# Optimization experiments

Measured on AMD Instinct MI355X. Metric: run time of the kernel, lower is better.

Reference implementation:

```python
import jax, jax.numpy as jnp
import numpy as np

D_MODEL, N_HEADS, WINDOW, N_STATE = 1024, 16, 256, 128
B, T = 2, 2048
EPS = 1e-5


def _layernorm(x, g, b):
    mu = jnp.mean(x, axis=-1, keepdims=True)
    var = jnp.mean((x - mu) ** 2, axis=-1, keepdims=True)
    return (x - mu) * jax.lax.rsqrt(var + EPS) * g + b


def setup_inputs() -> dict:
    key = jax.random.key(0)
    ks = jax.random.split(key, 20)
    d, h = D_MODEL, 4 * D_MODEL
    s = lambda k, *shape: jax.random.normal(k, shape, jnp.float32) * 0.02
    return {
        "x": jax.random.normal(ks[0], (B, T, d), jnp.float32),
        "ssm_state": jnp.zeros((B, N_STATE), jnp.float32),
        "ln1_g": jnp.ones((d,), jnp.float32), "ln1_b": jnp.zeros((d,), jnp.float32),
        "wq": s(ks[1], d, d), "bq": jnp.zeros((d,), jnp.float32),
        "wk": s(ks[2], d, d), "bk": jnp.zeros((d,), jnp.float32),
        "wv": s(ks[3], d, d), "bv": jnp.zeros((d,), jnp.float32),
        "wo": s(ks[4], d, d), "bo": jnp.zeros((d,), jnp.float32),
        "wg": s(ks[5], d, d), "bg": jnp.zeros((d,), jnp.float32),
        "A": jax.random.uniform(ks[6], (N_STATE,), jnp.float32, -0.1, 0.1),
        "Bw": s(ks[7], d, N_STATE),
        "Cw": s(ks[8], N_STATE, d),
        "ln2_g": jnp.ones((d,), jnp.float32), "ln2_b": jnp.zeros((d,), jnp.float32),
        "w1": s(ks[9], d, h), "b1": jnp.zeros((h,), jnp.float32),
        "w2": s(ks[10], h, d), "b2": jnp.zeros((d,), jnp.float32),
    }


def _forward(x, ssm_state, ln1_g, ln1_b, wq, bq, wk, bk, wv, bv, wo, bo,
             wg, bg, A, Bw, Cw, ln2_g, ln2_b, w1, b1, w2, b2):
    Bsz, Tlen, d = x.shape
    d_h = d // N_HEADS
    xn = _layernorm(x, ln1_g, ln1_b)

    # --- windowed causal attention (dense, per original) ---
    def heads(y):
        return y.reshape(Bsz, Tlen, N_HEADS, d_h).transpose(0, 2, 1, 3)
    Q = heads(xn @ wq + bq)
    K = heads(xn @ wk + bk)
    V = heads(xn @ wv + bv)
    scores = jnp.einsum("bhqd,bhkd->bhqk", Q, K) / (d_h ** 0.5)
    i = jnp.arange(Tlen)[:, None]
    j = jnp.arange(Tlen)[None, :]
    allowed = (j <= i) & (i - j < WINDOW)
    scores = jnp.where(allowed, scores, -jnp.inf)
    attn = jax.nn.softmax(scores, axis=-1)
    ao = jnp.einsum("bhqk,bhkd->bhqd", attn, V)
    ao = ao.transpose(0, 2, 1, 3).reshape(Bsz, Tlen, d)
    attn_out = ao @ wo + bo

    # --- diagonal SSM scan ---
    u = xn @ Bw  # (B,T,N)
    def step(s, u_t):
        s = A * s + u_t
        return s, s
    new_state, states = jax.lax.scan(step, ssm_state, u.transpose(1, 0, 2))
    ssm_out = states.transpose(1, 0, 2) @ Cw  # (B,T,d)

    # --- gated fusion + residual + MLP ---
    g = jax.nn.sigmoid(xn @ wg + bg)
    x = x + g * attn_out + (1.0 - g) * ssm_out
    xn2 = _layernorm(x, ln2_g, ln2_b)
    mlp = jax.nn.gelu(xn2 @ w1 + b1, approximate=False) @ w2 + b2
    return x + mlp, new_state


def reference(x, ssm_state, ln1_g, ln1_b, wq, bq, wk, bk, wv, bv, wo, bo,
              wg, bg, A, Bw, Cw, ln2_g, ln2_b, w1, b1, w2, b2):
    return _forward(x, ssm_state, ln1_g, ln1_b, wq, bq, wk, bk, wv, bv, wo, bo,
                    wg, bg, A, Bw, Cw, ln2_g, ln2_b, w1, b1, w2, b2)
```

## Files before the change

### kernel.cpp

```cpp
#include <hip/hip_runtime.h>

typedef __attribute__((ext_vector_type(8))) short bf16x8;
typedef __attribute__((ext_vector_type(4))) float f32x4;

#define D_MODEL 1024
#define T_LEN 2048
#define BATCH 2
#define N_HEADS 16
#define D_HEAD 64
#define WINDOW 256
#define N_STATE 128
#define D_FF 4096
#define N_CAT 4224
#define LDQ 4352
#define M_ROWS 4096

static __device__ __forceinline__ float bf2f(unsigned short u) {
  union { unsigned int i; float f; } v; v.i = ((unsigned int)u) << 16; return v.f;
}
static __device__ __forceinline__ unsigned short f2bf(float f) {
  unsigned int x = __float_as_uint(f);
  return (unsigned short)((x + 0x7FFFu + ((x >> 16) & 1u)) >> 16);
}

static __device__ __forceinline__ void gl_lds16(const void* g, void* l) {
  __builtin_amdgcn_global_load_lds(
      (const __attribute__((address_space(1))) unsigned int*)g,
      (__attribute__((address_space(3))) unsigned int*)l, 16, 0, 0);
}

__global__ __launch_bounds__(256) void transpose_cvt(
    const float* __restrict__ src, unsigned short* __restrict__ dst,
    int K, int N, int n_off, int ldd)
{
  __shared__ float tile[32][33];
  const int kt = blockIdx.x * 32, nt = blockIdx.y * 32;
  const int c = threadIdx.x & 31, r0 = threadIdx.x >> 5;
#pragma unroll
  for (int i = 0; i < 4; i++) {
    const int r = r0 + i * 8;
    tile[r][c] = src[(size_t)(kt + r) * N + nt + c];
  }
  __syncthreads();
#pragma unroll
  for (int i = 0; i < 4; i++) {
    const int r = r0 + i * 8;
    dst[(size_t)(n_off + nt + r) * ldd + kt + c] = f2bf(tile[c][r]);
  }
}

__global__ __launch_bounds__(256) void transpose5(
    const float* __restrict__ s0, const float* __restrict__ s1,
    const float* __restrict__ s2, const float* __restrict__ s3,
    const float* __restrict__ s4, unsigned short* __restrict__ dcat,
    unsigned short* __restrict__ dwo)
{
  __shared__ float tile[32][33];
  const int z = blockIdx.z;
  const float* src = (z == 0) ? s0 : (z == 1) ? s1 : (z == 2) ? s2 : (z == 3) ? s3 : s4;
  unsigned short* dst = (z < 4) ? dcat + (size_t)z * 1024 * 1024 : dwo;
  const int kt = blockIdx.x * 32, nt = blockIdx.y * 32;
  const int c = threadIdx.x & 31, r0 = threadIdx.x >> 5;
#pragma unroll
  for (int i = 0; i < 4; i++) {
    const int r = r0 + i * 8;
    tile[r][c] = src[(size_t)(kt + r) * 1024 + nt + c];
  }
  __syncthreads();
#pragma unroll
  for (int i = 0; i < 4; i++) {
    const int r = r0 + i * 8;
    dst[(size_t)(nt + r) * 1024 + kt + c] = f2bf(tile[c][r]);
  }
}

__global__ __launch_bounds__(256) void vtrans_kernel(
    const unsigned short* __restrict__ qkvgu, unsigned short* __restrict__ VT)
{
  __shared__ unsigned short tile[32][33];
  const int bh = blockIdx.z;
  const int b = bh >> 4, h = bh & 15;
  const int t0 = blockIdx.x * 32, d0 = blockIdx.y * 32;
  const int c = threadIdx.x & 31, r0 = threadIdx.x >> 5;
#pragma unroll
  for (int i = 0; i < 4; i++) {
    const int r = r0 + i * 8;
    tile[r][c] = qkvgu[((size_t)b * T_LEN + t0 + r) * LDQ + 2048 + h * 64 + d0 + c];
  }
  __syncthreads();
#pragma unroll
  for (int i = 0; i < 4; i++) {
    const int r = r0 + i * 8;
    VT[((size_t)bh * 64 + d0 + r) * T_LEN + t0 + c] = tile[c][r];
  }
}

__global__ __launch_bounds__(256) void build_bcat(
    const float* __restrict__ bq, const float* __restrict__ bk,
    const float* __restrict__ bv, const float* __restrict__ bg,
    float* __restrict__ bcat)
{
  const int i = blockIdx.x * 256 + threadIdx.x;
  if (i < LDQ) {
    float v = 0.0f;
    if (i < 1024)      v = bq[i];
    else if (i < 2048) v = bk[i - 1024];
    else if (i < 3072) v = bv[i - 2048];
    else if (i < 4096) v = bg[i - 3072];
    bcat[i] = v;
  }
}

__global__ __launch_bounds__(256) void ln_kernel(
    const float* __restrict__ x, const float* __restrict__ g,
    const float* __restrict__ b, unsigned short* __restrict__ out)
{
  const int row = blockIdx.x, tid = threadIdx.x;
  const float4 xv = ((const float4*)(x + (size_t)row * 1024))[tid];
  float s  = xv.x + xv.y + xv.z + xv.w;
  float s2 = xv.x * xv.x + xv.y * xv.y + xv.z * xv.z + xv.w * xv.w;
#pragma unroll
  for (int off = 32; off >= 1; off >>= 1) {
    s  += __shfl_down(s, off);
    s2 += __shfl_down(s2, off);
  }
  __shared__ float red[8];
  const int wave = tid >> 6;
  if ((tid & 63) == 0) { red[wave] = s; red[4 + wave] = s2; }
  __syncthreads();
  s  = red[0] + red[1] + red[2] + red[3];
  s2 = red[4] + red[5] + red[6] + red[7];
  const float mu = s * (1.0f / 1024.0f);
  const float rs = rsqrtf(s2 * (1.0f / 1024.0f) - mu * mu + 1e-5f);
  const float4 gv = ((const float4*)g)[tid];
  const float4 bv = ((const float4*)b)[tid];
  ushort4 o;
  o.x = f2bf((xv.x - mu) * rs * gv.x + bv.x);
  o.y = f2bf((xv.y - mu) * rs * gv.y + bv.y);
  o.z = f2bf((xv.z - mu) * rs * gv.z + bv.z);
  o.w = f2bf((xv.w - mu) * rs * gv.w + bv.w);
  ((ushort4*)(out + (size_t)row * 1024))[tid] = o;
}

template<int ACT, bool OUT_BF16, bool RESID>
__global__ __launch_bounds__(256, 4) void gemm_ho(
    const unsigned short* __restrict__ A, const unsigned short* __restrict__ BT,
    const float* __restrict__ bias, const float* __restrict__ resid,
    void* __restrict__ Cout, int ldc, int K, int nbx)
{
  __shared__ char As[16384];
  __shared__ char Bs[8192];
  const int nwg = gridDim.x;
  int bid = blockIdx.x;
  {
    const int q = nwg >> 3, r = nwg & 7, xx = bid & 7, o = bid >> 3;
    bid = (xx < r ? xx * (q + 1) : r * (q + 1) + (xx - r) * q) + o;
  }
  const int m0 = (bid % nbx) * 128;
  const int n0 = (bid / nbx) * 64;
  const int tid = threadIdx.x, lane = tid & 63, wave = tid >> 6;
  const int l15 = lane & 15, lg = lane >> 4;
  const int wm = (wave & 1) * 64, wn = (wave >> 1) * 32;
  f32x4 acc[4][2];
#pragma unroll
  for (int i = 0; i < 4; i++)
#pragma unroll
    for (int j = 0; j < 2; j++) acc[i][j] = (f32x4){0.f, 0.f, 0.f, 0.f};

  const char* srcA[4]; const char* srcB[2];
#pragma unroll
  for (int j = 0; j < 4; j++) {
    const int p = j * 4096 + tid * 16;
    const int R = p >> 7;
    const int cb = (p & 127) ^ ((R & 7) << 4);
    srcA[j] = (const char*)A + (size_t)(m0 + R) * (size_t)(K * 2) + cb;
    if (j < 2) srcB[j] = (const char*)BT + (size_t)(n0 + R) * (size_t)(K * 2) + cb;
  }

  const int NT = K >> 6;
  for (int t = 0; t < NT; ++t) {
    __syncthreads();
#pragma unroll
    for (int j = 0; j < 4; j++)
      gl_lds16(srcA[j] + (size_t)t * 128, As + j * 4096 + tid * 16);
#pragma unroll
    for (int j = 0; j < 2; j++)
      gl_lds16(srcB[j] + (size_t)t * 128, Bs + j * 4096 + tid * 16);
    __syncthreads();
    bf16x8 af[4][2], bfr[2][2];
#pragma unroll
    for (int mf = 0; mf < 4; mf++)
#pragma unroll
      for (int ks = 0; ks < 2; ks++) {
        const int R = wm + mf * 16 + l15;
        af[mf][ks] = *(const bf16x8*)(As + (R << 7) + ((ks * 64 + lg * 16) ^ ((R & 7) << 4)));
      }
#pragma unroll
    for (int nf = 0; nf < 2; nf++)
#pragma unroll
      for (int ks = 0; ks < 2; ks++) {
        const int R = wn + nf * 16 + l15;
        bfr[nf][ks] = *(const bf16x8*)(Bs + (R << 7) + ((ks * 64 + lg * 16) ^ ((R & 7) << 4)));
      }
#pragma unroll
    for (int mf = 0; mf < 4; mf++)
#pragma unroll
      for (int nf = 0; nf < 2; nf++)
#pragma unroll
        for (int ks = 0; ks < 2; ks++)
          acc[mf][nf] = __builtin_amdgcn_mfma_f32_16x16x32_bf16(
              af[mf][ks], bfr[nf][ks], acc[mf][nf], 0, 0, 0);
  }

  if (OUT_BF16) {
    __syncthreads();
    unsigned short (*Ct)[64] = (unsigned short(*)[64])As;
#pragma unroll
    for (int nf = 0; nf < 2; nf++) {
      const int col = wn + nf * 16 + l15;
      const float bv = bias ? bias[n0 + col] : 0.0f;
#pragma unroll
      for (int mf = 0; mf < 4; mf++) {
        const int rbase = wm + mf * 16 + lg * 4;
#pragma unroll
        for (int r = 0; r < 4; r++) {
          float v = acc[mf][nf][r] + bv;
          if (ACT == 2) v = 0.5f * v * (1.0f + erff(v * 0.70710678118654752f));
          Ct[rbase + r][col] = f2bf(v);
        }
      }
    }
    __syncthreads();
    unsigned short* Cb = (unsigned short*)Cout;
#pragma unroll
    for (int pass = 0; pass < 4; pass++) {
      const int idx = pass * 256 + tid;
      const int row = idx >> 3, c8 = (idx & 7) * 8;
      const uint4 d = *(const uint4*)&Ct[row][c8];
      *(uint4*)(Cb + (size_t)(m0 + row) * ldc + n0 + c8) = d;
    }
  } else {
#pragma unroll
    for (int nf = 0; nf < 2; nf++) {
      const int col = n0 + wn + nf * 16 + l15;
      const float bv = bias ? bias[col] : 0.0f;
#pragma unroll
      for (int mf = 0; mf < 4; mf++) {
        const int rbase = m0 + wm + mf * 16 + lg * 4;
#pragma unroll
        for (int r = 0; r < 4; r++) {
          float v = acc[mf][nf][r] + bv;
          if (ACT == 2) v = 0.5f * v * (1.0f + erff(v * 0.70710678118654752f));
          const size_t idx = (size_t)(rbase + r) * ldc + col;
          if (RESID) v += resid[idx];
          ((float*)Cout)[idx] = v;
        }
      }
    }
  }
}

__global__ __launch_bounds__(256) void attn_kernel(
    const unsigned short* __restrict__ qkvgu, const unsigned short* __restrict__ VT,
    unsigned short* __restrict__ ao)
{
  __shared__ float S[16][276];
  unsigned short* P = (unsigned short*)&S[0][0];

  const int bx = ((blockIdx.x & 7) << 4) | (blockIdx.x >> 3);
  const int q0 = bx * 16;
  const int h  = blockIdx.y;
  const int b  = blockIdx.z;
  const int tid = threadIdx.x, lane = tid & 63, wave = tid >> 6;
  const int l15 = lane & 15, lg = lane >> 4;
  const size_t rowbase = (size_t)b * T_LEN;

  {
    const unsigned short* qp = qkvgu + (rowbase + q0 + l15) * LDQ + h * 64 + lg * 8;
    const bf16x8 aq0 = *(const bf16x8*)qp;
    const bf16x8 aq1 = *(const bf16x8*)(qp + 32);
    for (int kt = wave; kt < 17; kt += 4) {
      const int kbase = q0 - 256 + kt * 16;
      const int krow = kbase + l15;
      const int krc = krow < 0 ? 0 : krow;
      const unsigned short* kp = qkvgu + (rowbase + krc) * LDQ + 1024 + h * 64 + lg * 8;
      const bf16x8 bk0 = *(const bf16x8*)kp;
      const bf16x8 bk1 = *(const bf16x8*)(kp + 32);
      f32x4 sacc = (f32x4){0.f, 0.f, 0.f, 0.f};
      sacc = __builtin_amdgcn_mfma_f32_16x16x32_bf16(aq0, bk0, sacc, 0, 0, 0);
      sacc = __builtin_amdgcn_mfma_f32_16x16x32_bf16(aq1, bk1, sacc, 0, 0, 0);
#pragma unroll
      for (int r = 0; r < 4; r++) {
        const int qi = q0 + lg * 4 + r;
        const int kj = kbase + l15;
        const bool ok = (kj >= 0) && (kj <= qi) && (qi - kj < WINDOW);
        S[lg * 4 + r][kt * 16 + l15] = ok ? sacc[r] * 0.125f : -1e30f;
      }
    }
  }
  __syncthreads();

  {
    const int q = tid >> 4, sub = tid & 15;
    float mx = -1e30f;
    for (int c = sub; c < 272; c += 16) mx = fmaxf(mx, S[q][c]);
#pragma unroll
    for (int off = 8; off >= 1; off >>= 1) mx = fmaxf(mx, __shfl_xor(mx, off));
    float sum = 0.f;
    for (int c = sub; c < 272; c += 16) sum += __expf(S[q][c] - mx);
#pragma unroll
    for (int off = 8; off >= 1; off >>= 1) sum += __shfl_xor(sum, off);
    const float inv = 1.0f / sum;
    unsigned short* Prow = P + q * 552;
    for (int c = sub; c < 288; c += 16) {
      const float pv = (c < 272) ? __expf(S[q][c] - mx) * inv : 0.0f;
      Prow[c] = f2bf(pv);
    }
  }
  __syncthreads();

  {
    f32x4 oacc = (f32x4){0.f, 0.f, 0.f, 0.f};
    const int dn = wave * 16 + l15;
    const unsigned short* vrow = VT + ((size_t)(b * 16 + h) * 64 + dn) * T_LEN;
#pragma unroll
    for (int ks = 0; ks < 9; ks++) {
      const bf16x8 pa = *(const bf16x8*)(P + l15 * 552 + ks * 32 + lg * 8);
      int t = q0 - 256 + ks * 32 + lg * 8;
      t = t < 0 ? 0 : (t > T_LEN - 8 ? T_LEN - 8 : t);
      const bf16x8 vb = *(const bf16x8*)(vrow + t);
      oacc = __builtin_amdgcn_mfma_f32_16x16x32_bf16(pa, vb, oacc, 0, 0, 0);
    }
#pragma unroll
    for (int r = 0; r < 4; r++)
      ao[(rowbase + q0 + lg * 4 + r) * D_MODEL + h * 64 + dn] = f2bf(oacc[r]);
  }
}

__global__ __launch_bounds__(512) void scan_kernel(
    const unsigned short* __restrict__ qkvgu, const float* __restrict__ Avec,
    const float* __restrict__ s0, unsigned short* __restrict__ states,
    float* __restrict__ out_state)
{
  __shared__ float finals[8][128];
  const int b = blockIdx.x;
  const int tid = threadIdx.x;
  const int c = tid >> 6;
  const int n0 = (tid & 63) * 2;
  const float a0 = Avec[n0], a1 = Avec[n0 + 1];
  float sv0 = (c == 0) ? s0[b * 128 + n0]     : 0.0f;
  float sv1 = (c == 0) ? s0[b * 128 + n0 + 1] : 0.0f;
  const size_t ubase = (size_t)b * T_LEN * LDQ + 4096 + n0;
  unsigned short* sp = states + (size_t)b * T_LEN * N_STATE + n0;
  const int t0 = c * 256;
#pragma unroll 8
  for (int t = t0; t < t0 + 256; t++) {
    const ushort2 u = *(const ushort2*)&qkvgu[ubase + (size_t)t * LDQ];
    sv0 = fmaf(a0, sv0, bf2f(u.x));
    sv1 = fmaf(a1, sv1, bf2f(u.y));
    ushort2 o; o.x = f2bf(sv0); o.y = f2bf(sv1);
    *(ushort2*)&sp[(size_t)t * N_STATE] = o;
  }
  finals[c][n0] = sv0;
  finals[c][n0 + 1] = sv1;
  if (c == 7) { out_state[b * 128 + n0] = sv0; out_state[b * 128 + n0 + 1] = sv1; }
  __syncthreads();
  if (c > 0) {
    const float c0 = finals[c - 1][n0];
    const float c1 = finals[c - 1][n0 + 1];
    float f0 = a0, f1 = a1;
    for (int t = t0; t < t0 + 256; t++) {
      if (f0 == 0.0f && f1 == 0.0f) break;
      ushort2 cur = *(ushort2*)&sp[(size_t)t * N_STATE];
      cur.x = f2bf(bf2f(cur.x) + f0 * c0);
      cur.y = f2bf(bf2f(cur.y) + f1 * c1);
      *(ushort2*)&sp[(size_t)t * N_STATE] = cur;
      f0 *= a0; f1 *= a1;
    }
  }
}

__global__ __launch_bounds__(256) void fusion_ln2_kernel(
    const float* __restrict__ x, const unsigned short* __restrict__ qkvgu,
    const unsigned short* __restrict__ attn, const unsigned short* __restrict__ ssm,
    const float* __restrict__ g2, const float* __restrict__ b2,
    float* __restrict__ out, unsigned short* __restrict__ xn2)
{
  const int row = blockIdx.x, tid = threadIdx.x;
  const size_t e4 = (size_t)row * 1024 + tid * 4;
  const float4 xv = *(const float4*)(x + e4);
  const ushort4 au = *(const ushort4*)(attn + e4);
  const ushort4 su = *(const ushort4*)(ssm + e4);
  const ushort4 gu = *(const ushort4*)(qkvgu + (size_t)row * LDQ + 3072 + tid * 4);
  float4 o;
  {
    const float ga = 1.0f / (1.0f + __expf(-bf2f(gu.x)));
    const float gb = 1.0f / (1.0f + __expf(-bf2f(gu.y)));
    const float gc = 1.0f / (1.0f + __expf(-bf2f(gu.z)));
    const float gd = 1.0f / (1.0f + __expf(-bf2f(gu.w)));
    o.x = xv.x + ga * bf2f(au.x) + (1.0f - ga) * bf2f(su.x);
    o.y = xv.y + gb * bf2f(au.y) + (1.0f - gb) * bf2f(su.y);
    o.z = xv.z + gc * bf2f(au.z) + (1.0f - gc) * bf2f(su.z);
    o.w = xv.w + gd * bf2f(au.w) + (1.0f - gd) * bf2f(su.w);
  }
  *(float4*)(out + e4) = o;

  float s  = o.x + o.y + o.z + o.w;
  float s2 = o.x * o.x + o.y * o.y + o.z * o.z + o.w * o.w;
#pragma unroll
  for (int off = 32; off >= 1; off >>= 1) {
    s  += __shfl_down(s, off);
    s2 += __shfl_down(s2, off);
  }
  __shared__ float red[8];
  const int wave = tid >> 6;
  if ((tid & 63) == 0) { red[wave] = s; red[4 + wave] = s2; }
  __syncthreads();
  s  = red[0] + red[1] + red[2] + red[3];
  s2 = red[4] + red[5] + red[6] + red[7];
  const float mu = s * (1.0f / 1024.0f);
  const float rs = rsqrtf(s2 * (1.0f / 1024.0f) - mu * mu + 1e-5f);
  const float4 gv = ((const float4*)g2)[tid];
  const float4 bv = ((const float4*)b2)[tid];
  ushort4 ov;
  ov.x = f2bf((o.x - mu) * rs * gv.x + bv.x);
  ov.y = f2bf((o.y - mu) * rs * gv.y + bv.y);
  ov.z = f2bf((o.z - mu) * rs * gv.z + bv.z);
  ov.w = f2bf((o.w - mu) * rs * gv.w + bv.w);
  ((ushort4*)(xn2 + (size_t)row * 1024))[tid] = ov;
}

extern "C" void kernel_launch(void* const* d_in, const int* in_sizes, int n_in,
                              void* d_out, int out_size, void* d_ws, size_t ws_size,
                              hipStream_t stream)
{
  const float* x     = (const float*)d_in[0];
  const float* ssm0  = (const float*)d_in[1];
  const float* ln1_g = (const float*)d_in[2];
  const float* ln1_b = (const float*)d_in[3];
  const float* wq    = (const float*)d_in[4];
  const float* bq    = (const float*)d_in[5];
  const float* wk    = (const float*)d_in[6];
  const float* bk    = (const float*)d_in[7];
  const float* wv    = (const float*)d_in[8];
  const float* bv    = (const float*)d_in[9];
  const float* wo    = (const float*)d_in[10];
  const float* bo    = (const float*)d_in[11];
  const float* wg    = (const float*)d_in[12];
  const float* bg    = (const float*)d_in[13];
  const float* Av    = (const float*)d_in[14];
  const float* Bw    = (const float*)d_in[15];
  const float* Cw    = (const float*)d_in[16];
  const float* ln2_g = (const float*)d_in[17];
  const float* ln2_b = (const float*)d_in[18];
  const float* w1    = (const float*)d_in[19];
  const float* b1    = (const float*)d_in[20];
  const float* w2    = (const float*)d_in[21];
  const float* b2    = (const float*)d_in[22];

  char* p = (char*)d_ws;
  auto take = [&](size_t bytes) { char* q = p; p += (bytes + 255) & ~(size_t)255; return q; };
  unsigned short* WcatT  = (unsigned short*)take((size_t)LDQ * 1024 * 2);
  unsigned short* woT    = (unsigned short*)take((size_t)1024 * 1024 * 2);
  unsigned short* CwT    = (unsigned short*)take((size_t)1024 * 128 * 2);
  unsigned short* w1T    = (unsigned short*)take((size_t)4096 * 1024 * 2);
  unsigned short* w2T    = (unsigned short*)take((size_t)1024 * 4096 * 2);
  float*          bcat   = (float*)take((size_t)LDQ * 4);
  unsigned short* xn     = (unsigned short*)take((size_t)M_ROWS * 1024 * 2);
  unsigned short* qkvgu  = (unsigned short*)take((size_t)M_ROWS * LDQ * 2);
  unsigned short* VT     = (unsigned short*)take((size_t)BATCH * N_HEADS * 64 * T_LEN * 2);
  unsigned short* ao     = (unsigned short*)take((size_t)M_ROWS * 1024 * 2);
  unsigned short* states = (unsigned short*)take((size_t)M_ROWS * N_STATE * 2);
  unsigned short* attn_o = (unsigned short*)take((size_t)M_ROWS * 1024 * 2);
  unsigned short* ssm_o  = (unsigned short*)take((size_t)M_ROWS * 1024 * 2);
  unsigned short* hbuf   = qkvgu;

  float* outx = (float*)d_out;
  float* out_state = outx + (size_t)M_ROWS * 1024;

  transpose5<<<dim3(32, 32, 5), 256, 0, stream>>>(wq, wk, wv, wg, wo, WcatT, woT);
  transpose_cvt<<<dim3(32, 4), 256, 0, stream>>>(Bw, WcatT, 1024, 128, 4096, 1024);
  transpose_cvt<<<dim3(4, 32), 256, 0, stream>>>(Cw, CwT, 128, 1024, 0, 128);
  transpose_cvt<<<dim3(32, 128), 256, 0, stream>>>(w1, w1T, 1024, 4096, 0, 1024);
  transpose_cvt<<<dim3(128, 32), 256, 0, stream>>>(w2, w2T, 4096, 1024, 0, 4096);
  build_bcat<<<17, 256, 0, stream>>>(bq, bk, bv, bg, bcat);

  ln_kernel<<<M_ROWS, 256, 0, stream>>>(x, ln1_g, ln1_b, xn);
  gemm_ho<0, true, false><<<32 * 68, 256, 0, stream>>>(
      xn, WcatT, bcat, nullptr, qkvgu, LDQ, 1024, 32);
  vtrans_kernel<<<dim3(64, 2, 32), 256, 0, stream>>>(qkvgu, VT);
  attn_kernel<<<dim3(128, 16, 2), 256, 0, stream>>>(qkvgu, VT, ao);
  scan_kernel<<<2, 512, 0, stream>>>(qkvgu, Av, ssm0, states, out_state);
  gemm_ho<0, true, false><<<32 * 16, 256, 0, stream>>>(
      ao, woT, bo, nullptr, attn_o, 1024, 1024, 32);
  gemm_ho<0, true, false><<<32 * 16, 256, 0, stream>>>(
      states, CwT, nullptr, nullptr, ssm_o, 1024, 128, 32);
  fusion_ln2_kernel<<<4096, 256, 0, stream>>>(
      x, qkvgu, attn_o, ssm_o, ln2_g, ln2_b, outx, xn);
  gemm_ho<2, true, false><<<32 * 64, 256, 0, stream>>>(
      xn, w1T, b1, nullptr, hbuf, 4096, 1024, 32);
  gemm_ho<0, false, true><<<32 * 16, 256, 0, stream>>>(
      hbuf, w2T, b2, outx, outx, 1024, 4096, 32);
}
```

Before: 332.6 us.

## Add 128x128-tile GEMM for QKV and FFN1, split SSM scan into 16 chunks

Adds a new GEMM kernel with 128x128 output tiles, 64x64 per-wave subtiles, XOR-swizzled LDS and an LDS-staged bf16 epilogue that gives coalesced 16-byte stores. It replaces the 128x64 GEMM for the wide QKV+gate+Bw projection and the GELU FFN1 projection, raising operand reuse and halving the number of workgroups, with M-grouped block ordering for L2 locality. The SSM scan now uses 1024 threads and 16 chunks of 128 timesteps instead of 8 of 256, which shortens the serial chain at the cost of more carry-fixup work. Larger tiles use more registers and LDS, so fewer workgroups fit per CU (launch bounds drop to 3).

Result: faster. 307.7 us (-7.5%).

```diff
diff --git a/kernel.cpp b/kernel.cpp
--- a/kernel.cpp
+++ b/kernel.cpp
@@ -140,6 +140,106 @@
   o.z = f2bf((xv.z - mu) * rs * gv.z + bv.z);
   o.w = f2bf((xv.w - mu) * rs * gv.w + bv.w);
   ((ushort4*)(out + (size_t)row * 1024))[tid] = o;
+}
+
+template<int ACT>
+__global__ __launch_bounds__(256, 3) void gemm128ho(
+    const unsigned short* __restrict__ A, const unsigned short* __restrict__ BT,
+    const float* __restrict__ bias, unsigned short* __restrict__ C,
+    int ldc, int K, int nby)
+{
+  __shared__ char smem[32768];
+  char* const As = smem;
+  char* const Bs = smem + 16384;
+  const int nwg = gridDim.x;
+  int bid = blockIdx.x;
+  {
+    const int q = nwg >> 3, r = nwg & 7, xx = bid & 7, o = bid >> 3;
+    bid = (xx < r ? xx * (q + 1) : r * (q + 1) + (xx - r) * q) + o;
+  }
+  const int per_group = 8 * nby;
+  const int grp = bid / per_group, rem = bid % per_group;
+  const int m0 = (grp * 8 + (rem & 7)) * 128;
+  const int n0 = (rem >> 3) * 128;
+
+  const int tid = threadIdx.x, lane = tid & 63, wave = tid >> 6;
+  const int l15 = lane & 15, lg = lane >> 4;
+  const int wm = (wave >> 1) * 64, wn = (wave & 1) * 64;
+  f32x4 acc[4][4];
+#pragma unroll
+  for (int i = 0; i < 4; i++)
+#pragma unroll
+    for (int j = 0; j < 4; j++) acc[i][j] = (f32x4){0.f, 0.f, 0.f, 0.f};
+
+  const char* srcA[4]; const char* srcB[4];
+#pragma unroll
+  for (int j = 0; j < 4; j++) {
+    const int p = j * 4096 + tid * 16;
+    const int R = p >> 7;
+    const int cb = (p & 127) ^ ((R & 7) << 4);
+    srcA[j] = (const char*)A  + (size_t)(m0 + R) * (size_t)(K * 2) + cb;
+    srcB[j] = (const char*)BT + (size_t)(n0 + R) * (size_t)(K * 2) + cb;
+  }
+
+  const int NT = K >> 6;
+  for (int t = 0; t < NT; ++t) {
+    __syncthreads();
+#pragma unroll
+    for (int j = 0; j < 4; j++) {
+      gl_lds16(srcA[j] + (size_t)t * 128, As + j * 4096 + tid * 16);
+      gl_lds16(srcB[j] + (size_t)t * 128, Bs + j * 4096 + tid * 16);
+    }
+    __syncthreads();
+    bf16x8 af[4][2], bfr[4][2];
+#pragma unroll
+    for (int mf = 0; mf < 4; mf++)
+#pragma unroll
+      for (int ks = 0; ks < 2; ks++) {
+        const int R = wm + mf * 16 + l15;
+        af[mf][ks] = *(const bf16x8*)(As + (R << 7) + ((ks * 64 + lg * 16) ^ ((R & 7) << 4)));
+      }
+#pragma unroll
+    for (int nf = 0; nf < 4; nf++)
+#pragma unroll
+      for (int ks = 0; ks < 2; ks++) {
+        const int R = wn + nf * 16 + l15;
+        bfr[nf][ks] = *(const bf16x8*)(Bs + (R << 7) + ((ks * 64 + lg * 16) ^ ((R & 7) << 4)));
+      }
+#pragma unroll
+    for (int mf = 0; mf < 4; mf++)
+#pragma unroll
+      for (int nf = 0; nf < 4; nf++)
+#pragma unroll
+        for (int ks = 0; ks < 2; ks++)
+          acc[mf][nf] = __builtin_amdgcn_mfma_f32_16x16x32_bf16(
+              af[mf][ks], bfr[nf][ks], acc[mf][nf], 0, 0, 0);
+  }
+
+  __syncthreads();
+  unsigned short (*Ct)[128] = (unsigned short(*)[128])smem;
+#pragma unroll
+  for (int nf = 0; nf < 4; nf++) {
+    const int col = wn + nf * 16 + l15;
+    const float bv = bias[n0 + col];
+#pragma unroll
+    for (int mf = 0; mf < 4; mf++) {
+      const int rbase = wm + mf * 16 + lg * 4;
+#pragma unroll
+      for (int r = 0; r < 4; r++) {
+        float v = acc[mf][nf][r] + bv;
+        if (ACT == 2) v = 0.5f * v * (1.0f + erff(v * 0.70710678118654752f));
+        Ct[rbase + r][col] = f2bf(v);
+      }
+    }
+  }
+  __syncthreads();
+#pragma unroll
+  for (int pass = 0; pass < 8; pass++) {
+    const int idx = pass * 256 + tid;
+    const int row = idx >> 4, c8 = (idx & 15) * 8;
+    const uint4 d = *(const uint4*)&Ct[row][c8];
+    *(uint4*)(C + (size_t)(m0 + row) * ldc + n0 + c8) = d;
+  }
 }
 
 template<int ACT, bool OUT_BF16, bool RESID>
@@ -337,12 +437,12 @@
   }
 }
 
-__global__ __launch_bounds__(512) void scan_kernel(
+__global__ __launch_bounds__(1024) void scan_kernel(
     const unsigned short* __restrict__ qkvgu, const float* __restrict__ Avec,
     const float* __restrict__ s0, unsigned short* __restrict__ states,
     float* __restrict__ out_state)
 {
-  __shared__ float finals[8][128];
+  __shared__ float finals[16][128];
   const int b = blockIdx.x;
   const int tid = threadIdx.x;
   const int c = tid >> 6;
@@ -352,9 +452,9 @@
   float sv1 = (c == 0) ? s0[b * 128 + n0 + 1] : 0.0f;
   const size_t ubase = (size_t)b * T_LEN * LDQ + 4096 + n0;
   unsigned short* sp = states + (size_t)b * T_LEN * N_STATE + n0;
-  const int t0 = c * 256;
+  const int t0 = c * 128;
 #pragma unroll 8
-  for (int t = t0; t < t0 + 256; t++) {
+  for (int t = t0; t < t0 + 128; t++) {
     const ushort2 u = *(const ushort2*)&qkvgu[ubase + (size_t)t * LDQ];
     sv0 = fmaf(a0, sv0, bf2f(u.x));
     sv1 = fmaf(a1, sv1, bf2f(u.y));
@@ -363,13 +463,13 @@
   }
   finals[c][n0] = sv0;
   finals[c][n0 + 1] = sv1;
-  if (c == 7) { out_state[b * 128 + n0] = sv0; out_state[b * 128 + n0 + 1] = sv1; }
+  if (c == 15) { out_state[b * 128 + n0] = sv0; out_state[b * 128 + n0 + 1] = sv1; }
   __syncthreads();
   if (c > 0) {
     const float c0 = finals[c - 1][n0];
     const float c1 = finals[c - 1][n0 + 1];
     float f0 = a0, f1 = a1;
-    for (int t = t0; t < t0 + 256; t++) {
+    for (int t = t0; t < t0 + 128; t++) {
       if (f0 == 0.0f && f1 == 0.0f) break;
       ushort2 cur = *(ushort2*)&sp[(size_t)t * N_STATE];
       cur.x = f2bf(bf2f(cur.x) + f0 * c0);
@@ -486,19 +586,17 @@
   build_bcat<<<17, 256, 0, stream>>>(bq, bk, bv, bg, bcat);
 
   ln_kernel<<<M_ROWS, 256, 0, stream>>>(x, ln1_g, ln1_b, xn);
-  gemm_ho<0, true, false><<<32 * 68, 256, 0, stream>>>(
-      xn, WcatT, bcat, nullptr, qkvgu, LDQ, 1024, 32);
+  gemm128ho<0><<<32 * 34, 256, 0, stream>>>(xn, WcatT, bcat, qkvgu, LDQ, 1024, 34);
   vtrans_kernel<<<dim3(64, 2, 32), 256, 0, stream>>>(qkvgu, VT);
   attn_kernel<<<dim3(128, 16, 2), 256, 0, stream>>>(qkvgu, VT, ao);
-  scan_kernel<<<2, 512, 0, stream>>>(qkvgu, Av, ssm0, states, out_state);
+  scan_kernel<<<2, 1024, 0, stream>>>(qkvgu, Av, ssm0, states, out_state);
   gemm_ho<0, true, false><<<32 * 16, 256, 0, stream>>>(
       ao, woT, bo, nullptr, attn_o, 1024, 1024, 32);
   gemm_ho<0, true, false><<<32 * 16, 256, 0, stream>>>(
       states, CwT, nullptr, nullptr, ssm_o, 1024, 128, 32);
   fusion_ln2_kernel<<<4096, 256, 0, stream>>>(
       x, qkvgu, attn_o, ssm_o, ln2_g, ln2_b, outx, xn);
-  gemm_ho<2, true, false><<<32 * 64, 256, 0, stream>>>(
-      xn, w1T, b1, nullptr, hbuf, 4096, 1024, 32);
+  gemm128ho<2><<<32 * 32, 256, 0, stream>>>(xn, w1T, b1, hbuf, 4096, 1024, 32);
   gemm_ho<0, false, true><<<32 * 16, 256, 0, stream>>>(
       hbuf, w2T, b2, outx, outx, 1024, 4096, 32);
 }
```
